# Kernel optimization log

Hardware: AMD Instinct MI355X
Metric: run time of the kernel (lower is better)

The kernel has to match this reference:

```python
import jax, jax.numpy as jnp
import numpy as np

B, D, E, NF, FD, H = 8192, 1024, 6, 32, 32, 256
MINK, MAXK = 1, 4

def _lin(a, w, b):
    return a @ w.T + b

def setup_inputs():
    key = jax.random.key(0)
    it = iter(jax.random.split(key, 60))
    def nrm(shape, s=0.02):
        return jax.random.normal(next(it), shape, jnp.float32) * s
    z = lambda *s: jnp.zeros(s, jnp.float32)
    return dict(
        x=jax.random.normal(next(it), (B, D), jnp.float32),
        esp_patterns=nrm((E, D), 1.0),
        sim_w1=nrm((D // 2, D)), sim_b1=z(D // 2),
        sim_w2=nrm((E, D // 2)), sim_b2=z(E),
        rout_w1=nrm((D // 2, D + E)), rout_b1=z(D // 2),
        rout_w2=nrm((E, D // 2)), rout_b2=z(E),
        kpred_w1=nrm((16, 6)), kpred_b1=z(16),
        kpred_w2=nrm((1, 16)), kpred_b2=z(1),
        sp_v_w=nrm((D, D)), sp_v_b=z(D),
        sp_o_w=nrm((D, D)), sp_o_b=z(D),
        sp_q1_w=nrm((D, D)), sp_q1_b=z(D),
        sp_q2_w=nrm((D, D)), sp_q2_b=z(D),
        de_w1=nrm((H, D)), de_b1=z(H),
        de_w2=nrm((D, H)), de_b2=z(D),
        de_g_w=nrm((D, D)), de_g_b=z(D),
        cf_in_w=nrm((3 * FD, FD)), cf_in_b=z(3 * FD),
        cf_o_w=nrm((FD, FD)), cf_o_b=z(FD),
        cf_f_w=nrm((FD, FD)), cf_f_b=z(FD),
        hf_w1=nrm((H, D)), hf_b1=z(H),
        hf_w2=nrm((D, H)), hf_b2=z(D),
        tc_w=nrm((4, 1, 3), 0.2), tc_b=z(4),
        tf_w=nrm((1, 4), 0.2), tf_b=z(1),
        lt_w1=nrm((H, D)), lt_b1=z(H),
        lt_w2=nrm((D, H)), lt_b2=z(D),
        op_w=nrm((D, D)), op_b=z(D),
    )

def reference(x, esp_patterns, sim_w1, sim_b1, sim_w2, sim_b2, rout_w1, rout_b1, rout_w2, rout_b2,
              kpred_w1, kpred_b1, kpred_w2, kpred_b2, sp_v_w, sp_v_b, sp_o_w, sp_o_b,
              sp_q1_w, sp_q1_b, sp_q2_w, sp_q2_b, de_w1, de_b1, de_w2, de_b2, de_g_w, de_g_b,
              cf_in_w, cf_in_b, cf_o_w, cf_o_b, cf_f_w, cf_f_b, hf_w1, hf_b1, hf_w2, hf_b2,
              tc_w, tc_b, tf_w, tf_b, lt_w1, lt_b1, lt_w2, lt_b2, op_w, op_b):
    # ---- FeatureAnalyzer ----
    sparsity = (x == 0).astype(jnp.float32).mean(-1)
    var_u = jnp.var(x, axis=-1, ddof=1)            # torch default unbiased var
    magnitude = jnp.abs(x).max(-1)
    norm = jnp.linalg.norm(x, axis=-1)
    mean = x.mean(-1, keepdims=True)
    std = jnp.sqrt(var_u[:, None] + 1e-8)
    skew = (((x - mean) / std) ** 3).mean(-1)
    s_abs = -jnp.sort(-jnp.abs(x), axis=-1)        # descending
    top20 = int(0.2 * D)
    conc = s_abs[:, :top20].sum(-1) / (s_abs.sum(-1) + 1e-8)
    feats = jnp.stack([sparsity, var_u, magnitude, norm, skew, conc], -1)  # (B,6)
    # ---- IntelligentRouter ----
    spec = jax.nn.sigmoid(x @ esp_patterns.T + _lin(jax.nn.relu(_lin(x, sim_w1, sim_b1)), sim_w2, sim_b2))
    probs = jax.nn.softmax(_lin(jax.nn.relu(_lin(jnp.concatenate([x, spec], -1), rout_w1, rout_b1)), rout_w2, rout_b2), -1)
    k_ratio = jax.nn.sigmoid(_lin(jax.nn.relu(_lin(feats, kpred_w1, kpred_b1)), kpred_w2, kpred_b2))[:, 0]
    k_vals = MINK + (MAXK - MINK) * k_ratio
    k = jnp.clip(jnp.floor(jnp.median(k_vals)), MINK, MAXK).astype(jnp.int32)  # int(median) truncation
    tp, ti = jax.lax.top_k(probs, MAXK)
    gmask = jnp.arange(MAXK) < k
    gates = jax.nn.softmax(jnp.where(gmask, tp, -jnp.inf), -1)  # (B,MAXK)
    # ---- experts (eval mode: dropout = identity) ----
    # SparseQuadraticExpert: seq-len-1 MHA collapses to V->out projections
    att = _lin(_lin(x, sp_v_w, sp_v_b), sp_o_w, sp_o_b)
    e_sp = _lin(jax.nn.relu(_lin(att * x, sp_q1_w, sp_q1_b)), sp_q2_w, sp_q2_b)
    # DenseQuadraticExpert
    e_de = _lin(jax.nn.relu(_lin(x, de_w1, de_b1)), de_w2, de_b2) + jax.nn.sigmoid(_lin(x, de_g_w, de_g_b)) * x
    # CrossFieldQuadraticExpert: single-head attention over fields
    xf = x.reshape(-1, NF, FD)
    q, kk, v = jnp.split(_lin(xf, cf_in_w, cf_in_b), 3, axis=-1)
    attn = jax.nn.softmax(jnp.einsum('bqd,bkd->bqk', q, kk) / jnp.sqrt(jnp.float32(FD)), -1)
    att_f = _lin(jnp.einsum('bqk,bkd->bqd', attn, v), cf_o_w, cf_o_b)
    e_cf = _lin(att_f * xf, cf_f_w, cf_f_b).reshape(-1, D)
    # HighFreqQuadraticExpert
    filt = _lin(jnp.tanh(_lin(x, hf_w1, hf_b1)), hf_w2, hf_b2)
    e_hf = x + (filt - x) * x
    # TemporalQuadraticExpert (AdaptiveAvgPool1d(D) on length-D input == identity)
    conv = jax.nn.relu(jax.lax.conv_general_dilated(x[:, None, :], tc_w, (1,), [(1, 1)], dimension_numbers=('NCH', 'OIH', 'NCH')) + tc_b[None, :, None])
    wts = jax.nn.sigmoid(_lin(conv.transpose(0, 2, 1), tf_w, tf_b))[..., 0]  # (B,D)
    e_tp = (x * wts) * x
    # LongTailQuadraticExpert
    t = _lin(jax.nn.elu(_lin(x, lt_w1, lt_b1)), lt_w2, lt_b2)
    e_lt = jnp.sign(x) * jnp.sqrt(jnp.abs(t * x) + 1e-8)
    # ---- dispatch + combine ----
    stack = jnp.stack([e_sp, e_de, e_cf, e_hf, e_tp, e_lt], axis=1)  # (B,E,D)
    sel = jnp.take_along_axis(stack, ti[:, :, None], axis=1)         # (B,MAXK,D)
    comb = (gates[:, :, None] * sel).sum(1)
    return _lin(comb, op_w, op_b) + x  # output projection + residual; Identity norm (batch_norm=False)
```

## Files before the change

### kernel.cpp

```cpp
#include <hip/hip_runtime.h>
#include <stdint.h>

typedef unsigned short u16;
typedef __attribute__((ext_vector_type(2))) float f32x2;
typedef __attribute__((ext_vector_type(4))) float f32x4;
typedef __attribute__((ext_vector_type(4))) unsigned short u16x4;
typedef __attribute__((ext_vector_type(8))) short short8;

#define DEV static __device__ __forceinline__

DEV float bf2f(u16 u){ union{unsigned int i; float f;} v; v.i=((unsigned int)u)<<16; return v.f; }
DEV u16 f2bf(float f){ union{float f; unsigned int i;} v; v.f=f; unsigned int u=v.i;
  return (u16)((u + 0x7FFFu + ((u>>16)&1u))>>16); }
DEV float wred(float v){ for(int o=32;o;o>>=1) v += __shfl_xor(v,o); return v; }
DEV float wredmax(float v){ for(int o=32;o;o>>=1) v = fmaxf(v,__shfl_xor(v,o)); return v; }
DEV int wredi(int v){ for(int o=32;o;o>>=1) v += __shfl_xor(v,o); return v; }

DEV void gload16(const void* g, void* l){
  __builtin_amdgcn_global_load_lds((const __attribute__((address_space(1))) unsigned int*)g,
                                   (__attribute__((address_space(3))) unsigned int*)l, 16, 0, 0);
}

DEV float actf(int ACT, float v){
  if(ACT==1) return v>0.f?v:0.f;
  if(ACT==2) return 1.f/(1.f+__expf(-v));
  if(ACT==3) return tanhf(v);
  if(ACT==4) return v>0.f?v:(__expf(v)-1.f);
  return v;
}

__global__ void cvt5_kernel(
    const float* __restrict__ s0, const float* __restrict__ s1, const float* __restrict__ s2,
    const float* __restrict__ s3, const float* __restrict__ s4,
    u16* __restrict__ d0, u16* __restrict__ d1, u16* __restrict__ d2,
    u16* __restrict__ d3, u16* __restrict__ d4, int n4each){
  const float* ss[5]={s0,s1,s2,s3,s4};
  u16* dd[5]={d0,d1,d2,d3,d4};
  const int total=5*n4each;
  for(int i=blockIdx.x*blockDim.x+threadIdx.x; i<total; i+=gridDim.x*blockDim.x){
    int b=i/n4each, r=i-b*n4each;
    f32x4 v=((const f32x4*)ss[b])[r];
    u16x4 o;
    #pragma unroll
    for(int j=0;j<4;++j) o[j]=f2bf(v[j]);
    ((u16x4*)dd[b])[r]=o;
  }
}

__global__ void cvt6_kernel(
    const float* __restrict__ s0, const float* __restrict__ s1, const float* __restrict__ s2,
    const float* __restrict__ s3, const float* __restrict__ s4, const float* __restrict__ s5,
    u16* __restrict__ d0, u16* __restrict__ d1, u16* __restrict__ d2,
    u16* __restrict__ d3, u16* __restrict__ d4, u16* __restrict__ d5, int n4each){
  const float* ss[6]={s0,s1,s2,s3,s4,s5};
  u16* dd[6]={d0,d1,d2,d3,d4,d5};
  const int total=6*n4each;
  for(int i=blockIdx.x*blockDim.x+threadIdx.x; i<total; i+=gridDim.x*blockDim.x){
    int b=i/n4each, r=i-b*n4each;
    f32x4 v=((const f32x4*)ss[b])[r];
    u16x4 o;
    #pragma unroll
    for(int j=0;j<4;++j) o[j]=f2bf(v[j]);
    ((u16x4*)dd[b])[r]=o;
  }
}

__global__ void cvt_split(const float* __restrict__ s, u16* __restrict__ hi, u16* __restrict__ lo, int n4){
  for(int i=blockIdx.x*blockDim.x+threadIdx.x; i<n4; i+=gridDim.x*blockDim.x){
    f32x4 v=((const f32x4*)s)[i];
    u16x4 h,l;
    #pragma unroll
    for(int j=0;j<4;++j){ h[j]=f2bf(v[j]); l[j]=f2bf(v[j]-bf2f(h[j])); }
    ((u16x4*)hi)[i]=h; ((u16x4*)lo)[i]=l;
  }
}

__global__ void cvt_split_rw1(const float* __restrict__ src, u16* __restrict__ hi, u16* __restrict__ lo){
  for(int i=blockIdx.x*blockDim.x+threadIdx.x; i<512*1024; i+=gridDim.x*blockDim.x){
    int r=i>>10, c=i&1023;
    float v=src[(size_t)r*1030+c];
    u16 h=f2bf(v);
    hi[i]=h; lo[i]=f2bf(v-bf2f(h));
  }
}

__global__ __launch_bounds__(256) void transpose_bf(const float* __restrict__ src, u16* __restrict__ dst){
  __shared__ float t[32][33];
  const int bx=blockIdx.x&31, by=blockIdx.x>>5;
  const int lx=threadIdx.x&31, ly=threadIdx.x>>5;
  #pragma unroll
  for(int r=0;r<4;++r)
    t[ly+8*r][lx] = src[(size_t)(by*32+ly+8*r)*1024 + bx*32+lx];
  __syncthreads();
  #pragma unroll
  for(int r=0;r<4;++r)
    dst[(size_t)(bx*32+ly+8*r)*1024 + by*32+lx] = f2bf(t[lx][ly+8*r]);
}

__global__ __launch_bounds__(256) void small_pack(
    const float* __restrict__ spo_w, const float* __restrict__ spv_b, const float* __restrict__ spo_b,
    const float* __restrict__ de_b1, const float* __restrict__ hf_b1, const float* __restrict__ lt_b1,
    const float* __restrict__ sim_b1, const float* __restrict__ rout_b1,
    const float* __restrict__ rout_w1,
    float* __restrict__ bc, float* __restrict__ b768, float* __restrict__ b1024,
    float* __restrict__ rw1t)
{
  const int b=blockIdx.x, tid=threadIdx.x;
  if(b<256){
    const int wv=tid>>6, lane=tid&63;
    const int rowi=b*4+wv;
    float s=0.f;
    const float* wr=spo_w+(size_t)rowi*1024;
    #pragma unroll
    for(int j=0;j<16;++j) s+=wr[j*64+lane]*spv_b[j*64+lane];
    s=wred(s);
    if(lane==0) bc[rowi]=spo_b[rowi]+s;
  } else if(b==256){
    for(int i=tid;i<768;i+=256){
      float v = (i<256)? de_b1[i] : (i<512? hf_b1[i-256] : lt_b1[i-512]);
      b768[i]=v;
    }
  } else if(b==257){
    for(int i=tid;i<1024;i+=256) b1024[i]= (i<512)? sim_b1[i] : rout_b1[i-512];
  } else {
    int base=(b-258)*1536;
    for(int t=tid;t<1536;t+=256){
      int i=base+t;
      if(i<3072){
        int e=i>>9, col=i&511;
        rw1t[i]=rout_w1[(size_t)col*1030+1024+e];
      }
    }
  }
}

template<int ACT, int EPI>
__global__ __launch_bounds__(256) void gemm_bt(
    const u16* __restrict__ A, const u16* __restrict__ W,
    const float* __restrict__ bias, const u16* __restrict__ auxb,
    const float* __restrict__ auxf, const float* __restrict__ wsel,
    u16* __restrict__ comb, void* __restrict__ Cv, const u16* __restrict__ auxh,
    int M, int N, int K, int lda)
{
  __shared__ __align__(16) u16 lA[128*64];
  __shared__ __align__(16) u16 lB[128*64];
  const int tid=threadIdx.x, lane=tid&63, wv=tid>>6;
  const int wr=wv>>1, wc=wv&1;
  const int gx=gridDim.x;
  const int nwg=gx*gridDim.y;
  const int flat=blockIdx.y*gx+blockIdx.x;
  const int chunk=nwg>>3;
  const int nf=(flat&7)*chunk + (flat>>3);
  const int bn=(nf%gx)*128, bm=(nf/gx)*128;
  f32x4 acc[4][4];
  #pragma unroll
  for(int m=0;m<4;++m){
    #pragma unroll
    for(int n=0;n<4;++n) acc[m][n]=(f32x4)0.f;
  }
  const int srow = wv*8 + (lane>>3);
  const int scol = (lane&7)*8;
  for(int kt=0;kt<K;kt+=64){
    #pragma unroll
    for(int i=0;i<4;++i){
      gload16(A + (size_t)(bm + i*32 + srow)*lda + kt + scol, &lA[(i*32 + wv*8)*64]);
      gload16(W + (size_t)(bn + i*32 + srow)*K + kt + scol, &lB[(i*32 + wv*8)*64]);
    }
    __syncthreads();
    #pragma unroll
    for(int kk=0;kk<2;++kk){
      const int fr=lane&15, kc=kk*32+(lane>>4)*8;
      short8 af[4], bfr[4];
      #pragma unroll
      for(int m=0;m<4;++m) af[m]=*(const short8*)&lA[(wr*64+m*16+fr)*64+kc];
      #pragma unroll
      for(int n=0;n<4;++n) bfr[n]=*(const short8*)&lB[(wc*64+n*16+fr)*64+kc];
      #pragma unroll
      for(int m=0;m<4;++m){
        #pragma unroll
        for(int n=0;n<4;++n)
          acc[m][n]=__builtin_amdgcn_mfma_f32_16x16x32_bf16(af[m],bfr[n],acc[m][n],0,0,0);
      }
    }
    __syncthreads();
  }
  const int fr=lane&15, fq=lane>>4;
  #pragma unroll
  for(int m=0;m<4;++m){
    #pragma unroll
    for(int n=0;n<4;++n){
      const int col = bn + wc*64 + n*16 + fr;
      const float bv = bias ? bias[col] : 0.f;
      #pragma unroll
      for(int j=0;j<4;++j){
        const int row = bm + wr*64 + m*16 + fq*4 + j;
        const size_t idx = (size_t)row*N+col;
        float v = acc[m][n][j] + bv;
        if(ACT==5){
          v = (col<256) ? fmaxf(v,0.f) : (col<512 ? tanhf(v) : (v>0.f?v:(__expf(v)-1.f)));
        } else v = actf(ACT, v);
        if(EPI==0){ ((u16*)Cv)[idx]=f2bf(v); }
        else if(EPI==1){ ((float*)Cv)[idx]=v; }
        else if(EPI==2){ ((u16*)Cv)[idx]=f2bf(v*bf2f(auxb[idx])); }
        else if(EPI==3){ comb[idx]=f2bf(wsel[row*6+0]*v); }
        else if(EPI==4){ comb[idx]=f2bf(bf2f(comb[idx])+wsel[row*6+1]*(v + bf2f(auxb[idx])*bf2f(auxh[idx]))); }
        else if(EPI==5){ float x0=bf2f(auxb[idx]); comb[idx]=f2bf(bf2f(comb[idx])+wsel[row*6+3]*(x0+(v-x0)*x0)); }
        else if(EPI==6){
          float x0=bf2f(auxb[idx]);
          float sg=(x0>0.f)?1.f:((x0<0.f)?-1.f:0.f);
          comb[idx]=f2bf(bf2f(comb[idx])+wsel[row*6+5]*sg*sqrtf(fabsf(v*x0)+1e-8f));
        }
        else { ((float*)Cv)[idx]=v+auxf[idx]; }
      }
    }
  }
}

__global__ __launch_bounds__(256) void gemm_split2(
    const u16* __restrict__ Ah, const u16* __restrict__ Al,
    const u16* __restrict__ Wh, const u16* __restrict__ Wl,
    const float* __restrict__ bias, float* __restrict__ C, int M, int N, int K)
{
  const int LDL=40;
  __shared__ __align__(16) u16 lAh[128*40], lAl[128*40], lBh[128*40], lBl[128*40];
  const int tid=threadIdx.x, lane=tid&63, wv=tid>>6;
  const int wr=wv>>1, wc=wv&1;
  const int nwg=gridDim.x;
  const int wg=(blockIdx.x%8)*(nwg/8)+blockIdx.x/8;
  const int bx=wg&7, by=wg>>3;
  const int bn=bx*128, bm=by*128;
  f32x4 acc[4][4];
  #pragma unroll
  for(int m=0;m<4;++m){
    #pragma unroll
    for(int n=0;n<4;++n) acc[m][n]=(f32x4)0.f;
  }
  const int srow=tid>>2, scol=(tid&3)*8;
  for(int kt=0;kt<K;kt+=32){
    short8 rah[2],ral[2],rbh[2],rbl[2];
    #pragma unroll
    for(int i=0;i<2;++i){
      size_t ao=(size_t)(bm+i*64+srow)*K+kt+scol;
      size_t bo=(size_t)(bn+i*64+srow)*K+kt+scol;
      rah[i]=*(const short8*)(Ah+ao); ral[i]=*(const short8*)(Al+ao);
      rbh[i]=*(const short8*)(Wh+bo); rbl[i]=*(const short8*)(Wl+bo);
    }
    __syncthreads();
    #pragma unroll
    for(int i=0;i<2;++i){
      int d=(i*64+srow)*LDL+scol;
      *(short8*)&lAh[d]=rah[i]; *(short8*)&lAl[d]=ral[i];
      *(short8*)&lBh[d]=rbh[i]; *(short8*)&lBl[d]=rbl[i];
    }
    __syncthreads();
    const int fr=lane&15, kc=(lane>>4)*8;
    short8 ah[4],al[4],bh[4],bl[4];
    #pragma unroll
    for(int m=0;m<4;++m){ int r=(wr*64+m*16+fr)*LDL+kc; ah[m]=*(const short8*)&lAh[r]; al[m]=*(const short8*)&lAl[r]; }
    #pragma unroll
    for(int n=0;n<4;++n){ int r=(wc*64+n*16+fr)*LDL+kc; bh[n]=*(const short8*)&lBh[r]; bl[n]=*(const short8*)&lBl[r]; }
    #pragma unroll
    for(int m=0;m<4;++m){
      #pragma unroll
      for(int n=0;n<4;++n){
        acc[m][n]=__builtin_amdgcn_mfma_f32_16x16x32_bf16(ah[m],bh[n],acc[m][n],0,0,0);
        acc[m][n]=__builtin_amdgcn_mfma_f32_16x16x32_bf16(ah[m],bl[n],acc[m][n],0,0,0);
        acc[m][n]=__builtin_amdgcn_mfma_f32_16x16x32_bf16(al[m],bh[n],acc[m][n],0,0,0);
      }
    }
  }
  const int fr=lane&15, fq=lane>>4;
  #pragma unroll
  for(int m=0;m<4;++m){
    #pragma unroll
    for(int n=0;n<4;++n){
      const int col = bn + wc*64 + n*16 + fr;
      const float bv = bias[col];
      #pragma unroll
      for(int j=0;j<4;++j){
        const int row = bm + wr*64 + m*16 + fq*4 + j;
        float v = acc[m][n][j] + bv;
        if(col<512) v=fmaxf(v,0.f);
        C[(size_t)row*N+col] = v;
      }
    }
  }
}

__global__ __launch_bounds__(256) void feats_kernel(const float* __restrict__ x,
    const float* __restrict__ kw1, const float* __restrict__ kb1,
    const float* __restrict__ kw2, const float* __restrict__ kb2,
    float* __restrict__ kvals, u16* __restrict__ x_hi, u16* __restrict__ x_lo)
{
  const int lane=threadIdx.x&63, wv=threadIdx.x>>6;
  const int row=blockIdx.x*4+wv;
  const float* xr=x+(size_t)row*1024;
  u16x4* hio=(u16x4*)(x_hi+(size_t)row*1024);
  u16x4* loo=(u16x4*)(x_lo+(size_t)row*1024);
  float xv[16]; unsigned int cd[16];
  float s=0.f, ss=0.f, sa=0.f, nz=0.f, amax=0.f;
  #pragma unroll
  for(int t=0;t<4;++t){
    f32x4 v=((const f32x4*)xr)[t*64+lane];
    u16x4 h,l;
    #pragma unroll
    for(int j=0;j<4;++j){
      float f=v[j];
      union{float f;unsigned int i;} c; c.f=f;
      xv[t*4+j]=f; cd[t*4+j]=c.i&0x7fffffffu;
      h[j]=f2bf(f); l[j]=f2bf(f-bf2f(h[j]));
      s+=f; ss+=f*f; float a=fabsf(f); sa+=a; amax=fmaxf(amax,a); if(f==0.f) nz+=1.f;
    }
    hio[t*64+lane]=h; loo[t*64+lane]=l;
  }
  s=wred(s); ss=wred(ss); sa=wred(sa); nz=wred(nz); amax=wredmax(amax);
  const float mean=s/1024.f;
  const float var=(ss - s*mean)/1023.f;
  const float inv=1.f/sqrtf(var+1e-8f);
  float sk=0.f;
  #pragma unroll
  for(int j=0;j<16;++j){ float z=(xv[j]-mean)*inv; sk+=z*z*z; }
  sk=wred(sk);
  unsigned int lo=0u, hi=0x7f800000u;
  while(hi-lo>1u){
    unsigned int mid=(lo+hi)>>1;
    int c=0;
    #pragma unroll
    for(int j=0;j<16;++j) c += (cd[j] >= mid);
    c=wredi(c);
    if(c>=204) lo=mid; else hi=mid;
  }
  const unsigned int T=lo;
  float sg=0.f, cg=0.f;
  #pragma unroll
  for(int j=0;j<16;++j){ if(cd[j] > T){ sg+=fabsf(xv[j]); cg+=1.f; } }
  sg=wred(sg); cg=wred(cg);
  if(lane==0){
    union{unsigned int i;float f;} tv; tv.i=T;
    float conc=(sg + (204.f-cg)*tv.f)/(sa + 1e-8f);
    float feats[6]={ nz/1024.f, var, amax, sqrtf(ss), sk/1024.f, conc };
    float out=kb2[0];
    #pragma unroll
    for(int i=0;i<16;++i){
      float hv=kb1[i];
      #pragma unroll
      for(int j=0;j<6;++j) hv+=kw1[i*6+j]*feats[j];
      hv=fmaxf(hv,0.f);
      out+=kw2[i]*hv;
    }
    kvals[row]=1.f + 3.f*(1.f/(1.f+__expf(-out)));
  }
}

__global__ __launch_bounds__(256) void median_kernel(const float* __restrict__ kvals, int* __restrict__ kint){
  __shared__ unsigned int v[8192];
  __shared__ int hist4[4*257];
  __shared__ unsigned int selT;
  __shared__ int selR;
  const int tid=threadIdx.x, lane=tid&63, wv=tid>>6;
  for(int i=tid;i<8192;i+=256){ union{float f;unsigned int u;} c; c.f=kvals[i]; v[i]=c.u; }
  __syncthreads();
  unsigned int res[2];
  for(int t=0;t<2;++t){
    int r = 8192 - (4096+t) + 1;
    unsigned int prefix=0u;
    for(int lvl=0;lvl<4;++lvl){
      const int shift=24-lvl*8;
      const unsigned int pmask = (lvl==0)?0u:(0xFFFFFFFFu<<(shift+8));
      for(int i=tid;i<4*257;i+=256) hist4[i]=0;
      __syncthreads();
      for(int i=tid;i<8192;i+=256){
        unsigned int c=v[i];
        if((c&pmask)==prefix) atomicAdd(&hist4[wv*257+((c>>shift)&0xFFu)],1);
      }
      __syncthreads();
      if(wv==0){
        int h[4]; int ls=0;
        #pragma unroll
        for(int b=0;b<4;++b){
          int bin=lane*4+b;
          h[b]=hist4[bin]+hist4[257+bin]+hist4[514+bin]+hist4[771+bin];
          ls+=h[b];
        }
        int pfx=ls;
        #pragma unroll
        for(int off=1;off<64;off<<=1){ int tt=__shfl_up(pfx,off); if(lane>=off) pfx+=tt; }
        int total=__shfl(pfx,63);
        int cgt = total - pfx;
        #pragma unroll
        for(int b=3;b>=0;--b){
          if(cgt < r && r <= cgt + h[b]){
            selT = prefix | ((unsigned int)(lane*4+b)<<shift);
            selR = r - cgt;
          }
          cgt += h[b];
        }
      }
      __syncthreads();
      prefix=selT; r=selR;
      __syncthreads();
    }
    res[t]=prefix;
  }
  if(tid==0){
    union{unsigned int u; float f;} a,b; a.u=res[0]; b.u=res[1];
    float med=0.5f*(a.f+b.f);
    int k=(int)floorf(med);
    k = k<1?1:(k>4?4:k);
    *kint=k;
  }
}

__global__ __launch_bounds__(256) void router_kernel(const float* __restrict__ x,
    const float* __restrict__ h, const float* __restrict__ esp,
    const float* __restrict__ w2s, const float* __restrict__ b2s,
    const float* __restrict__ rw1t, const float* __restrict__ w2r,
    const float* __restrict__ b2r, const int* __restrict__ kint,
    float* __restrict__ wsel)
{
  const int wv=threadIdx.x>>6, lane=threadIdx.x&63;
  const int row=blockIdx.x*4+wv;
  const float* xr=x+(size_t)row*1024;
  const float* hr=h+(size_t)row*1024;
  float xv[16], h0[8], h1[8];
  #pragma unroll
  for(int j=0;j<16;++j) xv[j]=xr[j*64+lane];
  #pragma unroll
  for(int j=0;j<8;++j){ h0[j]=hr[j*64+lane]; h1[j]=hr[512+j*64+lane]; }
  float spec[6];
  #pragma unroll
  for(int e=0;e<6;++e){
    float s=0.f;
    #pragma unroll
    for(int j=0;j<16;++j) s+=xv[j]*esp[e*1024+j*64+lane];
    #pragma unroll
    for(int j=0;j<8;++j) s+=h0[j]*w2s[e*512+j*64+lane];
    s=wred(s);
    spec[e]=1.f/(1.f+__expf(-(s+b2s[e])));
  }
  #pragma unroll
  for(int e=0;e<6;++e){
    const float se=spec[e];
    #pragma unroll
    for(int j=0;j<8;++j) h1[j]+=se*rw1t[e*512+j*64+lane];
  }
  #pragma unroll
  for(int j=0;j<8;++j) h1[j]=fmaxf(h1[j],0.f);
  float p[6];
  float m=-1e30f;
  #pragma unroll
  for(int e=0;e<6;++e){
    float s=0.f;
    #pragma unroll
    for(int j=0;j<8;++j) s+=h1[j]*w2r[e*512+j*64+lane];
    p[e]=wred(s)+b2r[e];
    m=fmaxf(m,p[e]);
  }
  float den=0.f;
  #pragma unroll
  for(int e=0;e<6;++e){ p[e]=__expf(p[e]-m); den+=p[e]; }
  float invd=1.f/den;
  #pragma unroll
  for(int e=0;e<6;++e) p[e]*=invd;
  if(lane==0){
    const int k=*kint;
    float w[6]={0,0,0,0,0,0};
    bool used[6]={false,false,false,false,false,false};
    int idx[4]; float val[4];
    #pragma unroll
    for(int j=0;j<4;++j){
      int bi=0; float bv=-1e30f;
      #pragma unroll
      for(int e=0;e<6;++e) if(!used[e] && p[e]>bv){ bv=p[e]; bi=e; }
      used[bi]=true; idx[j]=bi; val[j]=bv;
    }
    float mm=val[0], dd=0.f, g[4]={0,0,0,0};
    for(int j=0;j<k;++j){ g[j]=__expf(val[j]-mm); dd+=g[j]; }
    for(int j=0;j<k;++j) w[idx[j]]=g[j]/dd;
    float* o=&wsel[(size_t)row*6];
    o[0]=w[0]; o[1]=w[1]; o[2]=w[2]; o[3]=w[3]; o[4]=w[4]; o[5]=w[5];
  }
}

__global__ __launch_bounds__(256) void cf_kernel(const u16* __restrict__ xh,
    const float* __restrict__ w_in, const float* __restrict__ b_in,
    const float* __restrict__ w_o, const float* __restrict__ b_o,
    const float* __restrict__ w_f, const float* __restrict__ b_f,
    const float* __restrict__ wsel, u16* __restrict__ comb){
  __shared__ __align__(16) u16 smem[6400 + 4*5120];
  const int tid=threadIdx.x, wv=tid>>6, lane=tid&63;
  const int fr=lane&15, fq=lane>>4;
  for(int i=tid;i<5120;i+=256){
    float v=(i<3072)? w_in[i] : (i<4096? w_o[i-3072] : w_f[i-4096]);
    smem[(i>>5)*40 + (i&31)] = f2bf(v);
  }
  u16* wb   = smem + 6400 + wv*5120;
  u16* xbf  = wb;
  u16* bufA = wb + 1280;
  u16* bufB = bufA + 1280;
  u16* bufC = bufB + 1280;
  const int row = blockIdx.x*4 + wv;
  const u16* xr = xh + (size_t)row*1024;
  #pragma unroll
  for(int t=0;t<4;++t){
    u16x4 v = ((const u16x4*)xr)[t*64+lane];
    int e=(t*64+lane)*4;
    *(u16x4*)&xbf[(e>>5)*40 + (e&31)] = v;
  }
  __syncthreads();
  short8 xa[2];
  #pragma unroll
  for(int ft=0;ft<2;++ft) xa[ft]=*(const short8*)&xbf[(ft*16+fr)*40 + fq*8];
  f32x4 acc1[2][6];
  #pragma unroll
  for(int ct=0;ct<6;++ct){
    short8 wfrag=*(const short8*)&smem[(ct*16+fr)*40 + fq*8];
    #pragma unroll
    for(int ft=0;ft<2;++ft)
      acc1[ft][ct]=__builtin_amdgcn_mfma_f32_16x16x32_bf16(xa[ft],wfrag,(f32x4)0.f,0,0,0);
  }
  float bi[6];
  #pragma unroll
  for(int ct=0;ct<6;++ct) bi[ct]=b_in[ct*16+fr];
  #pragma unroll
  for(int ct=0;ct<6;++ct){
    #pragma unroll
    for(int ft=0;ft<2;++ft){
      #pragma unroll
      for(int j=0;j<4;++j){
        u16 h=f2bf(acc1[ft][ct][j]+bi[ct]);
        int rg=ft*16+fq*4+j, cg=ct*16+fr;
        if(cg<32)      bufA[rg*40+cg]=h;
        else if(cg<64) bufB[rg*40+(cg-32)]=h;
        else           bufC[(cg-64)*40+rg]=h;
      }
    }
  }
  short8 qa0=*(const short8*)&bufA[fr*40+fq*8];
  short8 qa1=*(const short8*)&bufA[(16+fr)*40+fq*8];
  short8 kb0=*(const short8*)&bufB[fr*40+fq*8];
  short8 kb1=*(const short8*)&bufB[(16+fr)*40+fq*8];
  f32x4 aS[2][2];
  aS[0][0]=__builtin_amdgcn_mfma_f32_16x16x32_bf16(qa0,kb0,(f32x4)0.f,0,0,0);
  aS[0][1]=__builtin_amdgcn_mfma_f32_16x16x32_bf16(qa0,kb1,(f32x4)0.f,0,0,0);
  aS[1][0]=__builtin_amdgcn_mfma_f32_16x16x32_bf16(qa1,kb0,(f32x4)0.f,0,0,0);
  aS[1][1]=__builtin_amdgcn_mfma_f32_16x16x32_bf16(qa1,kb1,(f32x4)0.f,0,0,0);
  const float scale=0.17677669529663687f;
  #pragma unroll
  for(int rt=0;rt<2;++rt){
    #pragma unroll
    for(int j=0;j<4;++j){
      float e0=aS[rt][0][j]*scale, e1=aS[rt][1][j]*scale;
      float m=fmaxf(e0,e1);
      #pragma unroll
      for(int o=1;o<16;o<<=1) m=fmaxf(m,__shfl_xor(m,o));
      e0=__expf(e0-m); e1=__expf(e1-m);
      float den=e0+e1;
      #pragma unroll
      for(int o=1;o<16;o<<=1) den+=__shfl_xor(den,o);
      float inv=1.f/den;
      bufA[(rt*16+fq*4+j)*40 + fr]      = f2bf(e0*inv);
      bufA[(rt*16+fq*4+j)*40 + 16+fr]   = f2bf(e1*inv);
    }
  }
  short8 pa0=*(const short8*)&bufA[fr*40+fq*8];
  short8 pa1=*(const short8*)&bufA[(16+fr)*40+fq*8];
  short8 vb0=*(const short8*)&bufC[fr*40+fq*8];
  short8 vb1=*(const short8*)&bufC[(16+fr)*40+fq*8];
  f32x4 aA[2][2];
  aA[0][0]=__builtin_amdgcn_mfma_f32_16x16x32_bf16(pa0,vb0,(f32x4)0.f,0,0,0);
  aA[0][1]=__builtin_amdgcn_mfma_f32_16x16x32_bf16(pa0,vb1,(f32x4)0.f,0,0,0);
  aA[1][0]=__builtin_amdgcn_mfma_f32_16x16x32_bf16(pa1,vb0,(f32x4)0.f,0,0,0);
  aA[1][1]=__builtin_amdgcn_mfma_f32_16x16x32_bf16(pa1,vb1,(f32x4)0.f,0,0,0);
  #pragma unroll
  for(int rt=0;rt<2;++rt)
    #pragma unroll
    for(int dt=0;dt<2;++dt)
      #pragma unroll
      for(int j=0;j<4;++j)
        bufB[(rt*16+fq*4+j)*40 + dt*16+fr]=f2bf(aA[rt][dt][j]);
  short8 aa0=*(const short8*)&bufB[fr*40+fq*8];
  short8 aa1=*(const short8*)&bufB[(16+fr)*40+fq*8];
  short8 ob0=*(const short8*)&smem[(96+fr)*40+fq*8];
  short8 ob1=*(const short8*)&smem[(112+fr)*40+fq*8];
  f32x4 aF[2][2];
  aF[0][0]=__builtin_amdgcn_mfma_f32_16x16x32_bf16(aa0,ob0,(f32x4)0.f,0,0,0);
  aF[0][1]=__builtin_amdgcn_mfma_f32_16x16x32_bf16(aa0,ob1,(f32x4)0.f,0,0,0);
  aF[1][0]=__builtin_amdgcn_mfma_f32_16x16x32_bf16(aa1,ob0,(f32x4)0.f,0,0,0);
  aF[1][1]=__builtin_amdgcn_mfma_f32_16x16x32_bf16(aa1,ob1,(f32x4)0.f,0,0,0);
  float bo[2]={b_o[fr], b_o[16+fr]};
  #pragma unroll
  for(int rt=0;rt<2;++rt){
    #pragma unroll
    for(int dt=0;dt<2;++dt){
      #pragma unroll
      for(int j=0;j<4;++j){
        int fld=rt*16+fq*4+j, d=dt*16+fr;
        float attf=aF[rt][dt][j]+bo[dt];
        bufC[fld*40+d]=f2bf(attf*bf2f(xbf[fld*40+d]));
      }
    }
  }
  short8 pr0=*(const short8*)&bufC[fr*40+fq*8];
  short8 pr1=*(const short8*)&bufC[(16+fr)*40+fq*8];
  short8 fb0=*(const short8*)&smem[(128+fr)*40+fq*8];
  short8 fb1=*(const short8*)&smem[(144+fr)*40+fq*8];
  f32x4 aE[2][2];
  aE[0][0]=__builtin_amdgcn_mfma_f32_16x16x32_bf16(pr0,fb0,(f32x4)0.f,0,0,0);
  aE[0][1]=__builtin_amdgcn_mfma_f32_16x16x32_bf16(pr0,fb1,(f32x4)0.f,0,0,0);
  aE[1][0]=__builtin_amdgcn_mfma_f32_16x16x32_bf16(pr1,fb0,(f32x4)0.f,0,0,0);
  aE[1][1]=__builtin_amdgcn_mfma_f32_16x16x32_bf16(pr1,fb1,(f32x4)0.f,0,0,0);
  float bff[2]={b_f[fr], b_f[16+fr]};
  const float w2=wsel[row*6+2];
  u16* cb=&comb[(size_t)row*1024];
  #pragma unroll
  for(int rt=0;rt<2;++rt){
    #pragma unroll
    for(int dt=0;dt<2;++dt){
      #pragma unroll
      for(int j=0;j<4;++j){
        int fld=rt*16+fq*4+j, d=dt*16+fr;
        u16 old=cb[fld*32+d];
        cb[fld*32+d]=f2bf(bf2f(old)+w2*(aE[rt][dt][j]+bff[dt]));
      }
    }
  }
}

__global__ __launch_bounds__(256) void tp_kernel(const float* __restrict__ x,
    const float* __restrict__ wsel, const u16* __restrict__ comb,
    const float* __restrict__ tcw, const float* __restrict__ tcb,
    const float* __restrict__ tfw, const float* __restrict__ tfb,
    u16* __restrict__ obf){
  __shared__ float xs[1026];
  const int row=blockIdx.x, tid=threadIdx.x;
  f32x4 u=((const f32x4*)(x+(size_t)row*1024))[tid];
  #pragma unroll
  for(int j=0;j<4;++j) xs[1+4*tid+j]=u[j];
  if(tid==0){ xs[0]=0.f; xs[1025]=0.f; }
  __syncthreads();
  const float w4=wsel[row*6+4];
  float tc[4][3], tb[4], tf[4];
  #pragma unroll
  for(int o=0;o<4;++o){
    #pragma unroll
    for(int kh=0;kh<3;++kh) tc[o][kh]=tcw[o*3+kh];
    tb[o]=tcb[o]; tf[o]=tfw[o];
  }
  const float tfb0=tfb[0];
  u16x4 cv=((const u16x4*)(comb+(size_t)row*1024))[tid];
  u16x4 ov;
  #pragma unroll
  for(int j=0;j<4;++j){
    const int d=4*tid+j;
    float pre=tfb0;
    #pragma unroll
    for(int o=0;o<4;++o){
      float c=tb[o]+tc[o][0]*xs[d]+tc[o][1]*xs[d+1]+tc[o][2]*xs[d+2];
      pre+=tf[o]*fmaxf(c,0.f);
    }
    float wt=1.f/(1.f+__expf(-pre));
    float xv=xs[1+d];
    ov[j]=f2bf(bf2f(cv[j])+w4*xv*xv*wt);
  }
  ((u16x4*)(obf+(size_t)row*1024))[tid]=ov;
}

extern "C" void kernel_launch(void* const* d_in, const int* in_sizes, int n_in,
                              void* d_out, int out_size, void* d_ws, size_t ws_size,
                              hipStream_t stream)
{
  const float* x     =(const float*)d_in[0];
  const float* esp   =(const float*)d_in[1];
  const float* sim_w1=(const float*)d_in[2],  *sim_b1=(const float*)d_in[3];
  const float* sim_w2=(const float*)d_in[4],  *sim_b2=(const float*)d_in[5];
  const float* rout_w1=(const float*)d_in[6], *rout_b1=(const float*)d_in[7];
  const float* rout_w2=(const float*)d_in[8], *rout_b2=(const float*)d_in[9];
  const float* kw1=(const float*)d_in[10], *kb1=(const float*)d_in[11];
  const float* kw2=(const float*)d_in[12], *kb2=(const float*)d_in[13];
  const float* spv_w=(const float*)d_in[14], *spv_b=(const float*)d_in[15];
  const float* spo_w=(const float*)d_in[16], *spo_b=(const float*)d_in[17];
  const float* spq1_w=(const float*)d_in[18], *spq1_b=(const float*)d_in[19];
  const float* spq2_w=(const float*)d_in[20], *spq2_b=(const float*)d_in[21];
  const float* de_w1=(const float*)d_in[22], *de_b1=(const float*)d_in[23];
  const float* de_w2=(const float*)d_in[24], *de_b2=(const float*)d_in[25];
  const float* de_gw=(const float*)d_in[26], *de_gb=(const float*)d_in[27];
  const float* cf_inw=(const float*)d_in[28], *cf_inb=(const float*)d_in[29];
  const float* cf_ow=(const float*)d_in[30], *cf_ob=(const float*)d_in[31];
  const float* cf_fw=(const float*)d_in[32], *cf_fb=(const float*)d_in[33];
  const float* hf_w1=(const float*)d_in[34], *hf_b1=(const float*)d_in[35];
  const float* hf_w2=(const float*)d_in[36], *hf_b2=(const float*)d_in[37];
  const float* tc_w=(const float*)d_in[38], *tc_b=(const float*)d_in[39];
  const float* tf_w=(const float*)d_in[40], *tf_b=(const float*)d_in[41];
  const float* lt_w1=(const float*)d_in[42], *lt_b1=(const float*)d_in[43];
  const float* lt_w2=(const float*)d_in[44], *lt_b2=(const float*)d_in[45];
  const float* op_w=(const float*)d_in[46], *op_b=(const float*)d_in[47];
  float* out=(float*)d_out;
  (void)in_sizes; (void)n_in; (void)out_size; (void)ws_size;

  constexpr int NB=8192;
  const size_t BD=(size_t)NB*1024;
  char* base=(char*)d_ws; size_t off=0;
  auto carve=[&](size_t n)->void*{ void* q=base+off; off+=(n+255)&~(size_t)255; return q; };
  u16*  comb =(u16*)carve(BD*2);
  u16*  bufA =(u16*)carve(BD*2);
  u16*  bufB =(u16*)carve(BD*2);
  u16*  x_hi =(u16*)carve(BD*2);
  u16*  x_lo =(u16*)carve(BD*2);
  float* h1024=(float*)carve(BD*4);
  u16*  h768 =(u16*)carve((size_t)NB*768*2);
  u16* w1024h=(u16*)carve((size_t)1024*1024*2);
  u16* w1024l=(u16*)carve((size_t)1024*1024*2);
  u16* spv_bf =(u16*)carve((size_t)1024*1024*2);
  u16* spo_bf =(u16*)carve((size_t)1024*1024*2);
  u16* spq1_bf=(u16*)carve((size_t)1024*1024*2);
  u16* spq2_bf=(u16*)carve((size_t)1024*1024*2);
  u16* w768_bf=(u16*)carve((size_t)768*1024*2);
  u16* dew2_bf=(u16*)carve((size_t)1024*256*2);
  u16* degw_bf=(u16*)carve((size_t)1024*1024*2);
  u16* hfw2_bf=(u16*)carve((size_t)1024*256*2);
  u16* ltw2_bf=(u16*)carve((size_t)1024*256*2);
  u16* opw_bf =(u16*)carve((size_t)1024*1024*2);
  u16* spvT_bf=(u16*)carve((size_t)1024*1024*2);
  float* bc   =(float*)carve((size_t)1024*4);
  float* b768 =(float*)carve((size_t)768*4);
  float* b1024=(float*)carve((size_t)1024*4);
  float* rw1t =(float*)carve((size_t)3072*4);
  float* wsel=(float*)carve((size_t)NB*6*4);
  float* kvals=(float*)carve((size_t)NB*4);
  int*   kint=(int*)carve(256);

  const dim3 blk(256);
  auto cgrid=[&](int n4)->dim3{ int g=(n4+255)/256; return dim3(g>2048?2048:g); };

  feats_kernel<<<dim3(2048),blk,0,stream>>>(x, kw1,kb1,kw2,kb2, kvals, x_hi, x_lo);
  median_kernel<<<dim3(1),blk,0,stream>>>(kvals, kint);

  cvt_split<<<cgrid(131072),blk,0,stream>>>(sim_w1, w1024h, w1024l, 131072);
  cvt_split_rw1<<<cgrid(131072),blk,0,stream>>>(rout_w1, w1024h+524288, w1024l+524288);
  cvt5_kernel<<<cgrid(5*262144),blk,0,stream>>>(spo_w,spq1_w,spq2_w,de_gw,op_w,
                                                spo_bf,spq1_bf,spq2_bf,degw_bf,opw_bf, 262144);
  cvt6_kernel<<<cgrid(6*65536),blk,0,stream>>>(de_w1,de_w2,hf_w1,hf_w2,lt_w1,lt_w2,
                                               w768_bf,dew2_bf,w768_bf+262144,hfw2_bf,w768_bf+524288,ltw2_bf, 65536);
  transpose_bf<<<dim3(1024),blk,0,stream>>>(spv_w, spvT_bf);
  small_pack<<<dim3(260),blk,0,stream>>>(spo_w, spv_b, spo_b, de_b1, hf_b1, lt_b1,
                                         sim_b1, rout_b1, rout_w1, bc, b768, b1024, rw1t);

  gemm_split2<<<dim3(512),blk,0,stream>>>(x_hi,x_lo, w1024h,w1024l, b1024, h1024, NB,1024,1024);
  router_kernel<<<dim3(2048),blk,0,stream>>>(x, h1024, esp, sim_w2, sim_b2, rw1t, rout_w2, rout_b2, kint, wsel);

  gemm_bt<0,0><<<dim3(8,8),blk,0,stream>>>(spo_bf, spvT_bf, nullptr, nullptr, nullptr, nullptr, nullptr, spv_bf, nullptr, 1024,1024,1024,1024);

  gemm_bt<0,2><<<dim3(8,64),blk,0,stream>>>(x_hi, spv_bf, bc, x_hi, nullptr, nullptr, nullptr, bufB, nullptr, NB,1024,1024,1024);
  gemm_bt<1,0><<<dim3(8,64),blk,0,stream>>>(bufB, spq1_bf, spq1_b, nullptr, nullptr, nullptr, nullptr, bufA, nullptr, NB,1024,1024,1024);
  gemm_bt<0,3><<<dim3(8,64),blk,0,stream>>>(bufA, spq2_bf, spq2_b, nullptr, nullptr, wsel, comb, nullptr, nullptr, NB,1024,1024,1024);

  gemm_bt<5,0><<<dim3(6,64),blk,0,stream>>>(x_hi, w768_bf, b768, nullptr, nullptr, nullptr, nullptr, h768, nullptr, NB,768,1024,1024);

  gemm_bt<2,0><<<dim3(8,64),blk,0,stream>>>(x_hi, degw_bf, de_gb, nullptr, nullptr, nullptr, nullptr, bufB, nullptr, NB,1024,1024,1024);
  gemm_bt<0,4><<<dim3(8,64),blk,0,stream>>>(h768, dew2_bf, de_b2, bufB, nullptr, wsel, comb, nullptr, x_hi, NB,1024,256,768);

  cf_kernel<<<dim3(2048),blk,0,stream>>>(x_hi, cf_inw, cf_inb, cf_ow, cf_ob, cf_fw, cf_fb, wsel, comb);

  gemm_bt<0,5><<<dim3(8,64),blk,0,stream>>>(h768+256, hfw2_bf, hf_b2, x_hi, nullptr, wsel, comb, nullptr, nullptr, NB,1024,256,768);

  gemm_bt<0,6><<<dim3(8,64),blk,0,stream>>>(h768+512, ltw2_bf, lt_b2, x_hi, nullptr, wsel, comb, nullptr, nullptr, NB,1024,256,768);

  tp_kernel<<<dim3(NB),blk,0,stream>>>(x, wsel, comb, tc_w, tc_b, tf_w, tf_b, bufB);

  gemm_bt<0,7><<<dim3(8,64),blk,0,stream>>>(bufB, opw_bf, op_b, nullptr, x, nullptr, nullptr, out, nullptr, NB,1024,1024,1024);
}
```

Measured before the change: 542.4 us.

## Fuse three expert second-layer GEMMs into one kernel with a combined epilogue

Replaces three separate K=256 GEMMs (dense, high-frequency, long-tail experts) with one kernel. It loops over the three K segments of a packed 1024x768 weight, keeps a running weighted delta in registers, and does a single read-modify-write of comb at the end. This drops two kernel launches and two full read-modify-write passes over the bf16 combine buffer. The cost is more registers for the extra delta accumulator, which may lower occupancy, and a new weight/bias packing layout.

```diff
diff --git a/kernel.cpp b/kernel.cpp
--- a/kernel.cpp
+++ b/kernel.cpp
@@ -47,21 +47,23 @@
   }
 }
 
-__global__ void cvt6_kernel(
+__global__ void cvt_trio768(
     const float* __restrict__ s0, const float* __restrict__ s1, const float* __restrict__ s2,
-    const float* __restrict__ s3, const float* __restrict__ s4, const float* __restrict__ s5,
-    u16* __restrict__ d0, u16* __restrict__ d1, u16* __restrict__ d2,
-    u16* __restrict__ d3, u16* __restrict__ d4, u16* __restrict__ d5, int n4each){
-  const float* ss[6]={s0,s1,s2,s3,s4,s5};
-  u16* dd[6]={d0,d1,d2,d3,d4,d5};
-  const int total=6*n4each;
+    const float* __restrict__ t0, const float* __restrict__ t1, const float* __restrict__ t2,
+    u16* __restrict__ w768, u16* __restrict__ wtrio){
+  const float* ss[6]={s0,s1,s2,t0,t1,t2};
+  const int total=6*65536;
   for(int i=blockIdx.x*blockDim.x+threadIdx.x; i<total; i+=gridDim.x*blockDim.x){
-    int b=i/n4each, r=i-b*n4each;
+    int b=i>>16, r=i&65535;
     f32x4 v=((const f32x4*)ss[b])[r];
     u16x4 o;
     #pragma unroll
     for(int j=0;j<4;++j) o[j]=f2bf(v[j]);
-    ((u16x4*)dd[b])[r]=o;
+    if(b<3) ((u16x4*)(w768+(size_t)b*262144))[r]=o;
+    else{
+      int n=r>>6, k4=r&63;
+      ((u16x4*)(wtrio+(size_t)n*768+(size_t)(b-3)*256))[k4]=o;
+    }
   }
 }
 
@@ -102,8 +104,9 @@
     const float* __restrict__ de_b1, const float* __restrict__ hf_b1, const float* __restrict__ lt_b1,
     const float* __restrict__ sim_b1, const float* __restrict__ rout_b1,
     const float* __restrict__ rout_w1,
+    const float* __restrict__ de_b2, const float* __restrict__ hf_b2, const float* __restrict__ lt_b2,
     float* __restrict__ bc, float* __restrict__ b768, float* __restrict__ b1024,
-    float* __restrict__ rw1t)
+    float* __restrict__ rw1t, float* __restrict__ btrio)
 {
   const int b=blockIdx.x, tid=threadIdx.x;
   if(b<256){
@@ -119,6 +122,9 @@
     for(int i=tid;i<768;i+=256){
       float v = (i<256)? de_b1[i] : (i<512? hf_b1[i-256] : lt_b1[i-512]);
       b768[i]=v;
+    }
+    for(int i=tid;i<1024;i+=256){
+      btrio[i]=de_b2[i]; btrio[1024+i]=hf_b2[i]; btrio[2048+i]=lt_b2[i];
     }
   } else if(b==257){
     for(int i=tid;i<1024;i+=256) b1024[i]= (i<512)? sim_b1[i] : rout_b1[i-512];
@@ -203,14 +209,104 @@
         else if(EPI==1){ ((float*)Cv)[idx]=v; }
         else if(EPI==2){ ((u16*)Cv)[idx]=f2bf(v*bf2f(auxb[idx])); }
         else if(EPI==3){ comb[idx]=f2bf(wsel[row*6+0]*v); }
-        else if(EPI==4){ comb[idx]=f2bf(bf2f(comb[idx])+wsel[row*6+1]*(v + bf2f(auxb[idx])*bf2f(auxh[idx]))); }
-        else if(EPI==5){ float x0=bf2f(auxb[idx]); comb[idx]=f2bf(bf2f(comb[idx])+wsel[row*6+3]*(x0+(v-x0)*x0)); }
-        else if(EPI==6){
-          float x0=bf2f(auxb[idx]);
-          float sg=(x0>0.f)?1.f:((x0<0.f)?-1.f:0.f);
-          comb[idx]=f2bf(bf2f(comb[idx])+wsel[row*6+5]*sg*sqrtf(fabsf(v*x0)+1e-8f));
+        else { ((float*)Cv)[idx]=v+auxf[idx]; }
+      }
+    }
+  }
+}
+
+__global__ __launch_bounds__(256) void gemm_trio(
+    const u16* __restrict__ A, const u16* __restrict__ W,
+    const float* __restrict__ btrio, const u16* __restrict__ gate,
+    const u16* __restrict__ xh, const float* __restrict__ wsel,
+    u16* __restrict__ comb)
+{
+  __shared__ __align__(16) u16 lA[128*64];
+  __shared__ __align__(16) u16 lB[128*64];
+  const int tid=threadIdx.x, lane=tid&63, wv=tid>>6;
+  const int wr=wv>>1, wc=wv&1;
+  const int gx=gridDim.x;
+  const int nwg=gx*gridDim.y;
+  const int flat=blockIdx.y*gx+blockIdx.x;
+  const int chunk=nwg>>3;
+  const int nf=(flat&7)*chunk + (flat>>3);
+  const int bn=(nf%gx)*128, bm=(nf/gx)*128;
+  const int srow = wv*8 + (lane>>3);
+  const int scol = (lane&7)*8;
+  const int fr=lane&15, fq=lane>>4;
+  f32x4 delta[4][4];
+  #pragma unroll
+  for(int m=0;m<4;++m){
+    #pragma unroll
+    for(int n=0;n<4;++n) delta[m][n]=(f32x4)0.f;
+  }
+  #pragma unroll
+  for(int seg=0;seg<3;++seg){
+    f32x4 acc[4][4];
+    #pragma unroll
+    for(int m=0;m<4;++m){
+      #pragma unroll
+      for(int n=0;n<4;++n) acc[m][n]=(f32x4)0.f;
+    }
+    for(int kt=seg*256;kt<seg*256+256;kt+=64){
+      #pragma unroll
+      for(int i=0;i<4;++i){
+        gload16(A + (size_t)(bm + i*32 + srow)*768 + kt + scol, &lA[(i*32 + wv*8)*64]);
+        gload16(W + (size_t)(bn + i*32 + srow)*768 + kt + scol, &lB[(i*32 + wv*8)*64]);
+      }
+      __syncthreads();
+      #pragma unroll
+      for(int kk=0;kk<2;++kk){
+        const int kc=kk*32+(lane>>4)*8;
+        short8 af[4], bfr[4];
+        #pragma unroll
+        for(int m=0;m<4;++m) af[m]=*(const short8*)&lA[(wr*64+m*16+fr)*64+kc];
+        #pragma unroll
+        for(int n=0;n<4;++n) bfr[n]=*(const short8*)&lB[(wc*64+n*16+fr)*64+kc];
+        #pragma unroll
+        for(int m=0;m<4;++m){
+          #pragma unroll
+          for(int n=0;n<4;++n)
+            acc[m][n]=__builtin_amdgcn_mfma_f32_16x16x32_bf16(af[m],bfr[n],acc[m][n],0,0,0);
         }
-        else { ((float*)Cv)[idx]=v+auxf[idx]; }
+      }
+      __syncthreads();
+    }
+    #pragma unroll
+    for(int m=0;m<4;++m){
+      #pragma unroll
+      for(int n=0;n<4;++n){
+        const int col = bn + wc*64 + n*16 + fr;
+        const float bv = btrio[seg*1024+col];
+        #pragma unroll
+        for(int j=0;j<4;++j){
+          const int row = bm + wr*64 + m*16 + fq*4 + j;
+          const size_t idx=(size_t)row*1024+col;
+          float v = acc[m][n][j] + bv;
+          float x0 = bf2f(xh[idx]);
+          if(seg==0){
+            float g=bf2f(gate[idx]);
+            delta[m][n][j] += wsel[row*6+1]*(v + g*x0);
+          } else if(seg==1){
+            delta[m][n][j] += wsel[row*6+3]*(x0 + (v-x0)*x0);
+          } else {
+            float sg=(x0>0.f)?1.f:((x0<0.f)?-1.f:0.f);
+            delta[m][n][j] += wsel[row*6+5]*sg*sqrtf(fabsf(v*x0)+1e-8f);
+          }
+        }
+      }
+    }
+  }
+  #pragma unroll
+  for(int m=0;m<4;++m){
+    #pragma unroll
+    for(int n=0;n<4;++n){
+      const int col = bn + wc*64 + n*16 + fr;
+      #pragma unroll
+      for(int j=0;j<4;++j){
+        const int row = bm + wr*64 + m*16 + fq*4 + j;
+        const size_t idx=(size_t)row*1024+col;
+        comb[idx]=f2bf(bf2f(comb[idx])+delta[m][n][j]);
       }
     }
   }
@@ -716,16 +812,15 @@
   u16* spq1_bf=(u16*)carve((size_t)1024*1024*2);
   u16* spq2_bf=(u16*)carve((size_t)1024*1024*2);
   u16* w768_bf=(u16*)carve((size_t)768*1024*2);
-  u16* dew2_bf=(u16*)carve((size_t)1024*256*2);
+  u16* wtrio  =(u16*)carve((size_t)1024*768*2);
   u16* degw_bf=(u16*)carve((size_t)1024*1024*2);
-  u16* hfw2_bf=(u16*)carve((size_t)1024*256*2);
-  u16* ltw2_bf=(u16*)carve((size_t)1024*256*2);
   u16* opw_bf =(u16*)carve((size_t)1024*1024*2);
   u16* spvT_bf=(u16*)carve((size_t)1024*1024*2);
   float* bc   =(float*)carve((size_t)1024*4);
   float* b768 =(float*)carve((size_t)768*4);
   float* b1024=(float*)carve((size_t)1024*4);
   float* rw1t =(float*)carve((size_t)3072*4);
+  float* btrio=(float*)carve((size_t)3072*4);
   float* wsel=(float*)carve((size_t)NB*6*4);
   float* kvals=(float*)carve((size_t)NB*4);
   int*   kint=(int*)carve(256);
@@ -740,11 +835,11 @@
   cvt_split_rw1<<<cgrid(131072),blk,0,stream>>>(rout_w1, w1024h+524288, w1024l+524288);
   cvt5_kernel<<<cgrid(5*262144),blk,0,stream>>>(spo_w,spq1_w,spq2_w,de_gw,op_w,
                                                 spo_bf,spq1_bf,spq2_bf,degw_bf,opw_bf, 262144);
-  cvt6_kernel<<<cgrid(6*65536),blk,0,stream>>>(de_w1,de_w2,hf_w1,hf_w2,lt_w1,lt_w2,
-                                               w768_bf,dew2_bf,w768_bf+262144,hfw2_bf,w768_bf+524288,ltw2_bf, 65536);
+  cvt_trio768<<<cgrid(6*65536),blk,0,stream>>>(de_w1,hf_w1,lt_w1, de_w2,hf_w2,lt_w2, w768_bf, wtrio);
   transpose_bf<<<dim3(1024),blk,0,stream>>>(spv_w, spvT_bf);
   small_pack<<<dim3(260),blk,0,stream>>>(spo_w, spv_b, spo_b, de_b1, hf_b1, lt_b1,
-                                         sim_b1, rout_b1, rout_w1, bc, b768, b1024, rw1t);
+                                         sim_b1, rout_b1, rout_w1, de_b2, hf_b2, lt_b2,
+                                         bc, b768, b1024, rw1t, btrio);
 
   gemm_split2<<<dim3(512),blk,0,stream>>>(x_hi,x_lo, w1024h,w1024l, b1024, h1024, NB,1024,1024);
   router_kernel<<<dim3(2048),blk,0,stream>>>(x, h1024, esp, sim_w2, sim_b2, rw1t, rout_w2, rout_b2, kint, wsel);
@@ -758,14 +853,11 @@
   gemm_bt<5,0><<<dim3(6,64),blk,0,stream>>>(x_hi, w768_bf, b768, nullptr, nullptr, nullptr, nullptr, h768, nullptr, NB,768,1024,1024);
 
   gemm_bt<2,0><<<dim3(8,64),blk,0,stream>>>(x_hi, degw_bf, de_gb, nullptr, nullptr, nullptr, nullptr, bufB, nullptr, NB,1024,1024,1024);
-  gemm_bt<0,4><<<dim3(8,64),blk,0,stream>>>(h768, dew2_bf, de_b2, bufB, nullptr, wsel, comb, nullptr, x_hi, NB,1024,256,768);
+
+  gemm_trio<<<dim3(8,64),blk,0,stream>>>(h768, wtrio, btrio, bufB, x_hi, wsel, comb);
 
   cf_kernel<<<dim3(2048),blk,0,stream>>>(x_hi, cf_inw, cf_inb, cf_ow, cf_ob, cf_fw, cf_fb, wsel, comb);
 
-  gemm_bt<0,5><<<dim3(8,64),blk,0,stream>>>(h768+256, hfw2_bf, hf_b2, x_hi, nullptr, wsel, comb, nullptr, nullptr, NB,1024,256,768);
-
-  gemm_bt<0,6><<<dim3(8,64),blk,0,stream>>>(h768+512, ltw2_bf, lt_b2, x_hi, nullptr, wsel, comb, nullptr, nullptr, NB,1024,256,768);
-
   tp_kernel<<<dim3(NB),blk,0,stream>>>(x, wsel, comb, tc_w, tc_b, tf_w, tf_b, bufB);
 
   gemm_bt<0,7><<<dim3(8,64),blk,0,stream>>>(bufB, opw_bf, op_b, nullptr, x, nullptr, nullptr, out, nullptr, NB,1024,1024,1024);
```

Result: slower. 581.6 us (+7.2%).
